# Kernel optimization log

Measured on AMD Instinct MI355X. Metric: run time of the kernel, lower is better.

## Reference

```python
import jax, jax.numpy as jnp
import numpy as np

B, F, T, K = 131072, 1024, 100, 32  # batch, num_features, num_trees, features per tree (sqrt(F))


def setup_inputs() -> dict:
    key = jax.random.key(0)
    kx, kw = jax.random.split(key)
    x = jax.random.normal(kx, (B, F), dtype=jnp.float32)
    # per-tree random feature selection without replacement (np.random.choice replace=False)
    rng = np.random.default_rng(0)
    idx = np.argsort(rng.random((T, F)), axis=1)[:, :K].astype(np.int32)
    feature_indices = jnp.asarray(idx)
    feature_thresholds = jnp.zeros((T, K), dtype=jnp.float32)  # lazy-init zeros in original
    feature_weights = jax.random.uniform(kw, (T, K), dtype=jnp.float32)  # torch.rand
    return {
        "x": x,
        "feature_indices": feature_indices,
        "feature_thresholds": feature_thresholds,
        "feature_weights": feature_weights,
    }


def reference(x, feature_indices, feature_thresholds, feature_weights):
    # Per tree t: ws_t = sum_k (x[:, idx[t,k]] - thr[t,k]) * w[t,k]
    # Equivalent fused form: scatter weights into a dense [T, F] matrix and do one GEMM,
    # with per-tree bias sum_k thr*w. scatter-add handles any duplicate indices identically
    # to the gather-then-sum formulation.
    T_, K_ = feature_indices.shape
    tree_ids = jnp.arange(T_, dtype=feature_indices.dtype)[:, None]  # [T,1]
    W_full = jnp.zeros((T_, x.shape[1]), dtype=x.dtype).at[tree_ids, feature_indices].add(feature_weights)
    bias = jnp.sum(feature_thresholds * feature_weights, axis=1)  # [T]
    ws = x @ W_full.T - bias[None, :]  # [B, T]
    p = jax.nn.sigmoid(ws)
    pm = jnp.mean(p, axis=1)  # mean over trees; mean(1-p) = 1 - mean(p)
    return jnp.stack([1.0 - pm, pm], axis=1)  # [B, 2]
```

## Files before the change

kernel.cpp:

```cpp
#include <hip/hip_runtime.h>
#include <math.h>

constexpr int Bn = 131072;
constexpr int Fn = 1024;
constexpr int Tn = 100;
constexpr int Kn = 32;

constexpr int TP  = 112;
constexpr int NF  = TP / 16;
constexpr int BK  = 64;
constexpr int NT  = Fn / BK;
constexpr int BM  = 128;
constexpr int MW  = 32;
constexpr int WPB = 4;
constexpr int BLOCK = 256;
constexpr int GRID  = Bn / BM;

typedef __attribute__((ext_vector_type(8))) short bf16x8;
typedef __attribute__((ext_vector_type(4))) float f32x4;

__device__ inline unsigned short f2bf(float f) {
    uint32_t u = __float_as_uint(f);
    return (unsigned short)((u + 0x7FFFu + ((u >> 16) & 1u)) >> 16);
}

__device__ inline bf16x8 cvt8(f32x4 lo, f32x4 hi) {
    bf16x8 v;
    v[0] = (short)f2bf(lo[0]); v[1] = (short)f2bf(lo[1]);
    v[2] = (short)f2bf(lo[2]); v[3] = (short)f2bf(lo[3]);
    v[4] = (short)f2bf(hi[0]); v[5] = (short)f2bf(hi[1]);
    v[6] = (short)f2bf(hi[2]); v[7] = (short)f2bf(hi[3]);
    return v;
}

__global__ __launch_bounds__(64)
void rf_prep(const int* __restrict__ fidx, const float* __restrict__ fthr,
             const float* __restrict__ fw,
             unsigned short* __restrict__ wt, float* __restrict__ bias)
{
    const int t    = blockIdx.x;
    const int lane = threadIdx.x;

    int4 z = make_int4(0, 0, 0, 0);
    int4* rowp = (int4*)(wt + (size_t)t * Fn);
    rowp[lane * 2 + 0] = z;
    rowp[lane * 2 + 1] = z;
    __syncthreads();

    float bsum = 0.f;
    if (t < Tn && lane < Kn) {
        const int   idx = fidx[t * Kn + lane];
        const float w   = fw[t * Kn + lane];
        const float th  = fthr[t * Kn + lane];
        wt[(size_t)t * Fn + idx] = f2bf(w);
        bsum = th * w;
    }
#pragma unroll
    for (int d = 1; d < 64; d <<= 1) bsum += __shfl_xor(bsum, d, 64);
    if (lane == 0) bias[t] = (t < Tn) ? bsum : 0.f;
}


#define NTLD8(T, A0,A1,A2,A3,A4,A5,A6,A7) do {                             \
    const char* _p = (const char*)paA + (size_t)(T) * 256;                 \
    A0 = __builtin_nontemporal_load((const f32x4*)(_p + 0 * 16384));       \
    A1 = __builtin_nontemporal_load((const f32x4*)(_p + 1 * 16384));       \
    A2 = __builtin_nontemporal_load((const f32x4*)(_p + 2 * 16384));       \
    A3 = __builtin_nontemporal_load((const f32x4*)(_p + 3 * 16384));       \
    A4 = __builtin_nontemporal_load((const f32x4*)(_p + 4 * 16384));       \
    A5 = __builtin_nontemporal_load((const f32x4*)(_p + 5 * 16384));       \
    A6 = __builtin_nontemporal_load((const f32x4*)(_p + 6 * 16384));       \
    A7 = __builtin_nontemporal_load((const f32x4*)(_p + 7 * 16384));       \
} while (0)

#define DSWR8(BUFB, A0,A1,A2,A3,A4,A5,A6,A7) do {                          \
    *(f32x4*)(lbase + (BUFB) + w0) = A0;                                   \
    *(f32x4*)(lbase + (BUFB) + w1) = A1;                                   \
    *(f32x4*)(lbase + (BUFB) + w2) = A2;                                   \
    *(f32x4*)(lbase + (BUFB) + w3) = A3;                                   \
    *(f32x4*)(lbase + (BUFB) + w4) = A4;                                   \
    *(f32x4*)(lbase + (BUFB) + w5) = A5;                                   \
    *(f32x4*)(lbase + (BUFB) + w6) = A6;                                   \
    *(f32x4*)(lbase + (BUFB) + w7) = A7;                                   \
} while (0)

#define LOADB(T) do {                                                      \
    const char* _q = (const char*)pbB + (size_t)(T) * 128;                 \
    B00 = *(const bf16x8*)(_q + 0 * 32768);                                \
    B01 = *(const bf16x8*)(_q + 1 * 32768);                                \
    B02 = *(const bf16x8*)(_q + 2 * 32768);                                \
    B03 = *(const bf16x8*)(_q + 3 * 32768);                                \
    B04 = *(const bf16x8*)(_q + 4 * 32768);                                \
    B05 = *(const bf16x8*)(_q + 5 * 32768);                                \
    B06 = *(const bf16x8*)(_q + 6 * 32768);                                \
    B10 = *(const bf16x8*)(_q + 0 * 32768 + 64);                           \
    B11 = *(const bf16x8*)(_q + 1 * 32768 + 64);                           \
    B12 = *(const bf16x8*)(_q + 2 * 32768 + 64);                           \
    B13 = *(const bf16x8*)(_q + 3 * 32768 + 64);                           \
    B14 = *(const bf16x8*)(_q + 4 * 32768 + 64);                           \
    B15 = *(const bf16x8*)(_q + 5 * 32768 + 64);                           \
    B16 = *(const bf16x8*)(_q + 6 * 32768 + 64);                           \
} while (0)

#define READF(M, KS, LO, HI, BUFB) do {                                    \
    const char* _b = lbase + (BUFB) + ((M) * 16 + r) * 256;                \
    LO = *(const f32x4*)(_b + ((((KS) * 8 + g2 + 0) ^ r) * 16));           \
    HI = *(const f32x4*)(_b + ((((KS) * 8 + g2 + 1) ^ r) * 16));           \
} while (0)

#define MFMAROW(AF, Ba,Bb,Bc,Bd,Be,Bf,Bg, a0,a1,a2,a3,a4,a5,a6) do {       \
    a0 = __builtin_amdgcn_mfma_f32_16x16x32_bf16(AF, Ba, a0, 0, 0, 0);     \
    a1 = __builtin_amdgcn_mfma_f32_16x16x32_bf16(AF, Bb, a1, 0, 0, 0);     \
    a2 = __builtin_amdgcn_mfma_f32_16x16x32_bf16(AF, Bc, a2, 0, 0, 0);     \
    a3 = __builtin_amdgcn_mfma_f32_16x16x32_bf16(AF, Bd, a3, 0, 0, 0);     \
    a4 = __builtin_amdgcn_mfma_f32_16x16x32_bf16(AF, Be, a4, 0, 0, 0);     \
    a5 = __builtin_amdgcn_mfma_f32_16x16x32_bf16(AF, Bf, a5, 0, 0, 0);     \
    a6 = __builtin_amdgcn_mfma_f32_16x16x32_bf16(AF, Bg, a6, 0, 0, 0);     \
} while (0)

#define PHASE(TC, CB, OB) do {                                             \
    LOADB(TC);                                                             \
    READF(0, 0, L0, L1, CB);                                               \
    READF(1, 0, L2, L3, CB);                                               \
    READF(0, 1, L4, L5, CB);                                               \
    READF(1, 1, L6, L7, CB);                                               \
    asm volatile("s_waitcnt vmcnt(14)" ::: "memory");   \
    DSWR8(OB, A0, A1, A2, A3, A4, A5, A6, A7);                             \
    if ((TC) + 2 < NT) NTLD8((TC) + 2, A0, A1, A2, A3, A4, A5, A6, A7);    \
    {                                                                      \
        bf16x8 _af;                                                        \
        _af = cvt8(L0, L1);                                                \
        MFMAROW(_af, B00, B01, B02, B03, B04, B05, B06,                    \
                acc00, acc01, acc02, acc03, acc04, acc05, acc06);          \
        _af = cvt8(L2, L3);                                                \
        MFMAROW(_af, B00, B01, B02, B03, B04, B05, B06,                    \
                acc10, acc11, acc12, acc13, acc14, acc15, acc16);          \
        _af = cvt8(L4, L5);                                                \
        MFMAROW(_af, B10, B11, B12, B13, B14, B15, B16,                    \
                acc00, acc01, acc02, acc03, acc04, acc05, acc06);          \
        _af = cvt8(L6, L7);                                                \
        MFMAROW(_af, B10, B11, B12, B13, B14, B15, B16,                    \
                acc10, acc11, acc12, acc13, acc14, acc15, acc16);          \
    }                                                                      \
} while (0)

__global__ __launch_bounds__(BLOCK)
void rf_gemm(const float* __restrict__ x,
             const unsigned short* __restrict__ wt,
             const float* __restrict__ bias,
             float* __restrict__ out)
{
    __shared__ float lds[WPB][2][MW * BK];

    const int lane = threadIdx.x & 63;
    const int wid  = threadIdx.x >> 6;
    const int rb   = blockIdx.x * BM;
    const int r    = lane & 15;
    const int g    = lane >> 4;
    const int g2   = g * 2;
    const int sub  = lane >> 4;
    const int c    = lane & 15;

    const char* paA = (const char*)(x + (size_t)(rb + wid * MW + sub) * Fn) + c * 16;
    const char* pbB = (const char*)(wt + (size_t)r * Fn + g * 8);
    char* lbase = (char*)&lds[wid][0][0];

    const int w0 = (0 * 4 + sub) * 256 + ((c ^ ((0 * 4 + sub) & 15)) * 16);
    const int w1 = (1 * 4 + sub) * 256 + ((c ^ ((1 * 4 + sub) & 15)) * 16);
    const int w2 = (2 * 4 + sub) * 256 + ((c ^ ((2 * 4 + sub) & 15)) * 16);
    const int w3 = (3 * 4 + sub) * 256 + ((c ^ ((3 * 4 + sub) & 15)) * 16);
    const int w4 = (4 * 4 + sub) * 256 + ((c ^ ((4 * 4 + sub) & 15)) * 16);
    const int w5 = (5 * 4 + sub) * 256 + ((c ^ ((5 * 4 + sub) & 15)) * 16);
    const int w6 = (6 * 4 + sub) * 256 + ((c ^ ((6 * 4 + sub) & 15)) * 16);
    const int w7 = (7 * 4 + sub) * 256 + ((c ^ ((7 * 4 + sub) & 15)) * 16);

    f32x4 acc00 = {0,0,0,0}, acc01 = {0,0,0,0}, acc02 = {0,0,0,0},
          acc03 = {0,0,0,0}, acc04 = {0,0,0,0}, acc05 = {0,0,0,0},
          acc06 = {0,0,0,0};
    f32x4 acc10 = {0,0,0,0}, acc11 = {0,0,0,0}, acc12 = {0,0,0,0},
          acc13 = {0,0,0,0}, acc14 = {0,0,0,0}, acc15 = {0,0,0,0},
          acc16 = {0,0,0,0};

    f32x4 A0, A1, A2, A3, A4, A5, A6, A7;
    f32x4 L0, L1, L2, L3, L4, L5, L6, L7;
    bf16x8 B00, B01, B02, B03, B04, B05, B06;
    bf16x8 B10, B11, B12, B13, B14, B15, B16;

    NTLD8(0, A0, A1, A2, A3, A4, A5, A6, A7);
    DSWR8(0, A0, A1, A2, A3, A4, A5, A6, A7);
    NTLD8(1, A0, A1, A2, A3, A4, A5, A6, A7);

    for (int t = 0; t < NT; t += 2) {
        PHASE(t, 0, 8192);
        PHASE(t + 1, 8192, 0);
    }

    f32x4 accA[2][NF] = {
        { acc00, acc01, acc02, acc03, acc04, acc05, acc06 },
        { acc10, acc11, acc12, acc13, acc14, acc15, acc16 }
    };

    const int col = lane & 15;
    float psum[2][4] = {};
#pragma unroll
    for (int f = 0; f < NF; ++f) {
        const int  n     = f * 16 + col;
        const bool valid = n < Tn;
        const float bv   = bias[n];
#pragma unroll
        for (int m = 0; m < 2; ++m)
#pragma unroll
            for (int q = 0; q < 4; ++q) {
                const float ws = accA[m][f][q] - bv;
                const float p  = 1.f / (1.f + __expf(-ws));
                if (valid) psum[m][q] += p;
            }
    }
#pragma unroll
    for (int m = 0; m < 2; ++m)
#pragma unroll
        for (int q = 0; q < 4; ++q)
#pragma unroll
            for (int d = 1; d < 16; d <<= 1)
                psum[m][q] += __shfl_xor(psum[m][q], d, 64);

#pragma unroll
    for (int m = 0; m < 2; ++m) {
        if (col < 4) {
            const int q   = col;
            const int row = rb + wid * MW + m * 16 + g * 4 + q;
            const float pm = psum[m][q] * (1.0f / Tn);
            *(float2*)(out + (size_t)row * 2) = make_float2(1.0f - pm, pm);
        }
    }
}

extern "C" void kernel_launch(void* const* d_in, const int* in_sizes, int n_in,
                              void* d_out, int out_size, void* d_ws, size_t ws_size,
                              hipStream_t stream) {
    const float* x    = (const float*)d_in[0];
    const int*   fidx = (const int*)  d_in[1];
    const float* fthr = (const float*)d_in[2];
    const float* fw   = (const float*)d_in[3];
    float*       out  = (float*)d_out;

    unsigned short* wt   = (unsigned short*)d_ws;
    float*          bias = (float*)((char*)d_ws + (size_t)TP * Fn * 2);

    rf_prep<<<TP, 64, 0, stream>>>(fidx, fthr, fw, wt, bias);
    rf_gemm<<<GRID, BLOCK, 0, stream>>>(x, wt, bias, out);
}
```

Measured before the change: 152.4 us.

## Double-buffer global A staging registers and raise MFMA priority

The global loads for tile t+2 now go into a second set of staging registers and are issued at the start of each phase, before the B loads and LDS reads, instead of after the LDS write. The wait threshold becomes vmcnt(22), and the LDS write of the previously loaded tile is skipped once no next tile exists. s_setprio is raised around the MFMA block so the matrix work is favoured over other waves. This deepens the memory prefetch so the HBM-bound x stream stays in flight longer, at the cost of 32 extra VGPRs per thread, which may reduce occupancy.

```diff
diff --git a/kernel.cpp b/kernel.cpp
--- a/kernel.cpp
+++ b/kernel.cpp
@@ -61,31 +61,31 @@
 }
 
 
-#define NTLD8(T, A0,A1,A2,A3,A4,A5,A6,A7) do {                             \
-    const char* _p = (const char*)paA + (size_t)(T) * 256;                 \
-    A0 = __builtin_nontemporal_load((const f32x4*)(_p + 0 * 16384));       \
-    A1 = __builtin_nontemporal_load((const f32x4*)(_p + 1 * 16384));       \
-    A2 = __builtin_nontemporal_load((const f32x4*)(_p + 2 * 16384));       \
-    A3 = __builtin_nontemporal_load((const f32x4*)(_p + 3 * 16384));       \
-    A4 = __builtin_nontemporal_load((const f32x4*)(_p + 4 * 16384));       \
-    A5 = __builtin_nontemporal_load((const f32x4*)(_p + 5 * 16384));       \
-    A6 = __builtin_nontemporal_load((const f32x4*)(_p + 6 * 16384));       \
-    A7 = __builtin_nontemporal_load((const f32x4*)(_p + 7 * 16384));       \
-} while (0)
-
-#define DSWR8(BUFB, A0,A1,A2,A3,A4,A5,A6,A7) do {                          \
-    *(f32x4*)(lbase + (BUFB) + w0) = A0;                                   \
-    *(f32x4*)(lbase + (BUFB) + w1) = A1;                                   \
-    *(f32x4*)(lbase + (BUFB) + w2) = A2;                                   \
-    *(f32x4*)(lbase + (BUFB) + w3) = A3;                                   \
-    *(f32x4*)(lbase + (BUFB) + w4) = A4;                                   \
-    *(f32x4*)(lbase + (BUFB) + w5) = A5;                                   \
-    *(f32x4*)(lbase + (BUFB) + w6) = A6;                                   \
-    *(f32x4*)(lbase + (BUFB) + w7) = A7;                                   \
+#define NTLD8(T, S) do {                                                   \
+    const char* _p = paA + (size_t)(T) * 256;                              \
+    S##0 = __builtin_nontemporal_load((const f32x4*)(_p + 0 * 16384));     \
+    S##1 = __builtin_nontemporal_load((const f32x4*)(_p + 1 * 16384));     \
+    S##2 = __builtin_nontemporal_load((const f32x4*)(_p + 2 * 16384));     \
+    S##3 = __builtin_nontemporal_load((const f32x4*)(_p + 3 * 16384));     \
+    S##4 = __builtin_nontemporal_load((const f32x4*)(_p + 4 * 16384));     \
+    S##5 = __builtin_nontemporal_load((const f32x4*)(_p + 5 * 16384));     \
+    S##6 = __builtin_nontemporal_load((const f32x4*)(_p + 6 * 16384));     \
+    S##7 = __builtin_nontemporal_load((const f32x4*)(_p + 7 * 16384));     \
+} while (0)
+
+#define DSWR8(BUFB, S) do {                                                \
+    *(f32x4*)(lbase + (BUFB) + w0) = S##0;                                 \
+    *(f32x4*)(lbase + (BUFB) + w1) = S##1;                                 \
+    *(f32x4*)(lbase + (BUFB) + w2) = S##2;                                 \
+    *(f32x4*)(lbase + (BUFB) + w3) = S##3;                                 \
+    *(f32x4*)(lbase + (BUFB) + w4) = S##4;                                 \
+    *(f32x4*)(lbase + (BUFB) + w5) = S##5;                                 \
+    *(f32x4*)(lbase + (BUFB) + w6) = S##6;                                 \
+    *(f32x4*)(lbase + (BUFB) + w7) = S##7;                                 \
 } while (0)
 
 #define LOADB(T) do {                                                      \
-    const char* _q = (const char*)pbB + (size_t)(T) * 128;                 \
+    const char* _q = pbB + (size_t)(T) * 128;                              \
     B00 = *(const bf16x8*)(_q + 0 * 32768);                                \
     B01 = *(const bf16x8*)(_q + 1 * 32768);                                \
     B02 = *(const bf16x8*)(_q + 2 * 32768);                                \
@@ -118,15 +118,16 @@
     a6 = __builtin_amdgcn_mfma_f32_16x16x32_bf16(AF, Bg, a6, 0, 0, 0);     \
 } while (0)
 
-#define PHASE(TC, CB, OB) do {                                             \
+#define PHASE(TC, CB, OB, W, I) do {                                       \
+    if ((TC) + 2 < NT) NTLD8((TC) + 2, I);                                 \
     LOADB(TC);                                                             \
     READF(0, 0, L0, L1, CB);                                               \
     READF(1, 0, L2, L3, CB);                                               \
     READF(0, 1, L4, L5, CB);                                               \
     READF(1, 1, L6, L7, CB);                                               \
-    asm volatile("s_waitcnt vmcnt(14)" ::: "memory");   \
-    DSWR8(OB, A0, A1, A2, A3, A4, A5, A6, A7);                             \
-    if ((TC) + 2 < NT) NTLD8((TC) + 2, A0, A1, A2, A3, A4, A5, A6, A7);    \
+    asm volatile("s_waitcnt vmcnt(22)" ::: "memory");   \
+    if ((TC) + 1 < NT) DSWR8(OB, W);                                       \
+    __builtin_amdgcn_s_setprio(1);                                         \
     {                                                                      \
         bf16x8 _af;                                                        \
         _af = cvt8(L0, L1);                                                \
@@ -142,6 +143,7 @@
         MFMAROW(_af, B10, B11, B12, B13, B14, B15, B16,                    \
                 acc10, acc11, acc12, acc13, acc14, acc15, acc16);          \
     }                                                                      \
+    __builtin_amdgcn_s_setprio(0);                                         \
 } while (0)
 
 __global__ __launch_bounds__(BLOCK)
@@ -181,18 +183,19 @@
           acc13 = {0,0,0,0}, acc14 = {0,0,0,0}, acc15 = {0,0,0,0},
           acc16 = {0,0,0,0};
 
-    f32x4 A0, A1, A2, A3, A4, A5, A6, A7;
+    f32x4 SA0, SA1, SA2, SA3, SA4, SA5, SA6, SA7;
+    f32x4 SB0, SB1, SB2, SB3, SB4, SB5, SB6, SB7;
     f32x4 L0, L1, L2, L3, L4, L5, L6, L7;
     bf16x8 B00, B01, B02, B03, B04, B05, B06;
     bf16x8 B10, B11, B12, B13, B14, B15, B16;
 
-    NTLD8(0, A0, A1, A2, A3, A4, A5, A6, A7);
-    DSWR8(0, A0, A1, A2, A3, A4, A5, A6, A7);
-    NTLD8(1, A0, A1, A2, A3, A4, A5, A6, A7);
+    NTLD8(0, SA);
+    DSWR8(0, SA);
+    NTLD8(1, SB);
 
     for (int t = 0; t < NT; t += 2) {
-        PHASE(t, 0, 8192);
-        PHASE(t + 1, 8192, 0);
+        PHASE(t,     0,    8192, SB, SA);
+        PHASE(t + 1, 8192, 0,    SA, SB);
     }
 
     f32x4 accA[2][NF] = {
```

After: 166.8 us. 9.5% more time.
